# Kernel optimization log

Measured on AMD Instinct MI355X. Metric: run time of the kernel, lower is better.

The kernel has to match this reference:

```python
import jax, jax.numpy as jnp
import numpy as np

BINS = 100
ALPHA = 0.1

def entropy_batch(h):
    # Faithful to torch: histogram path is detached (done in numpy in original).
    h = jax.lax.stop_gradient(h)
    B, D = h.shape
    hp = h - jnp.min(h, axis=1, keepdims=True)
    hn = hp / jnp.max(hp, axis=1, keepdims=True)  # normalized to [0, 1]
    # np.histogram with `bins` uniform bins over [0,1]; rightmost edge inclusive -> clip
    idx = jnp.clip(jnp.floor(hn * BINS).astype(jnp.int32), 0, BINS - 1)
    rows = jnp.arange(B)[:, None]
    counts = jnp.zeros((B, BINS), jnp.float32).at[rows, idx].add(1.0)
    px = counts / jnp.float32(D)
    safe = jnp.where(px > 0, px, 1.0)
    ent = -jnp.sum(px * jnp.log(safe), axis=1) + jnp.log(jnp.float32(BINS))
    return jnp.mean(ent)

def setup_inputs() -> dict:
    key = jax.random.key(0)
    ks = jax.random.split(key, 8)
    B = 65536
    archi = [246, 246, 246, 246, 246, 246]
    dims = [784] + archi
    inp = {"x": jax.random.normal(ks[0], (B, 1, 28, 28), jnp.float32)}
    for i in range(6):
        inp[f"W{i+1}"] = 0.01 * jax.random.normal(ks[i + 1], (dims[i + 1], dims[i]), jnp.float32)
        inp[f"b{i+1}"] = jnp.zeros((dims[i + 1],), jnp.float32)
    inp["W7"] = 0.01 * jax.random.normal(ks[7], (10, archi[-1]), jnp.float32)
    inp["b7"] = jnp.zeros((10,), jnp.float32)
    return inp

def reference(x, W1, b1, W2, b2, W3, b3, W4, b4, W5, b5, W6, b6, W7, b7):
    h = x.reshape(-1, 784)
    Hs = []
    for W, b in ((W1, b1), (W2, b2), (W3, b3), (W4, b4), (W5, b5), (W6, b6)):
        h = jax.nn.leaky_relu(h @ W.T + b, negative_slope=ALPHA)
        Hs.append(entropy_batch(h))
    logits = jax.nn.relu(h @ W7.T + b7)
    out = jax.nn.log_softmax(logits, axis=1)
    return (out, Hs[0], Hs[1], Hs[2], Hs[3], Hs[4], Hs[5])
```

## Files before the change

kernel.cpp:

```cpp
#include <hip/hip_runtime.h>
#include <cstdint>
#include <cmath>

#define BATCH 65536
#define NREAL 246
#define NPAD  256
#define K1    784
#define K1PAD 832
#define BINS  100
#define ALPHA 0.1f
#define RB    128
#define NBLK  (BATCH/RB)

typedef __bf16 bf16x8 __attribute__((ext_vector_type(8)));
typedef __bf16 bf16x4 __attribute__((ext_vector_type(4)));
typedef float  f32x4  __attribute__((ext_vector_type(4)));

__global__ __launch_bounds__(256)
void pad_weights(const float* __restrict__ W1, const float* __restrict__ W2,
                 const float* __restrict__ W3, const float* __restrict__ W4,
                 const float* __restrict__ W5, const float* __restrict__ W6,
                 const float* __restrict__ W7,
                 __bf16* __restrict__ W1p, __bf16* __restrict__ Wp,
                 __bf16* __restrict__ W7p)
{
    int tid = blockIdx.x * 256 + threadIdx.x;
    const int n1 = NPAD * K1PAD;
    const int n2 = 5 * NPAD * NPAD;
    if (tid < n1) {
        int row = tid / K1PAD;
        int k   = tid - row * K1PAD;
        W1p[tid] = (__bf16)((row < NREAL && k < K1) ? W1[row * K1 + k] : 0.0f);
    } else if (tid < n1 + n2) {
        int t = tid - n1;
        int wsel = t >> 16;
        int idx  = t & 65535;
        int row  = idx >> 8, k = idx & 255;
        const float* W = (wsel == 0) ? W2 : (wsel == 1) ? W3 : (wsel == 2) ? W4
                        : (wsel == 3) ? W5 : W6;
        Wp[t] = (__bf16)((row < NREAL && k < NREAL) ? W[row * NREAL + k] : 0.0f);
    } else if (tid < n1 + n2 + 16 * NPAD) {
        int t = tid - n1 - n2;
        int row = t >> 8, k = t & 255;
        W7p[t] = (__bf16)((row < 10 && k < NREAL) ? W7[row * NREAL + k] : 0.0f);
    }
}

__global__ __launch_bounds__(512)
void mega(const float* __restrict__ x,
          const __bf16* __restrict__ W1p,
          const __bf16* __restrict__ Wp,
          const __bf16* __restrict__ W7p,
          const float* __restrict__ b1, const float* __restrict__ b2,
          const float* __restrict__ b3, const float* __restrict__ b4,
          const float* __restrict__ b5, const float* __restrict__ b6,
          const float* __restrict__ b7,
          float* __restrict__ out, float* __restrict__ partial)
{
    __shared__ __bf16 Hs[RB * NPAD];
    __shared__ char   aux[32768];
    char* Hb = (char*)Hs;

    const int tid = threadIdx.x;
    const int w = tid >> 6, l = tid & 63;
    const int lane16 = l & 15, lane4 = l >> 4;
    const int wr = (w >> 2) * 64;
    const int wc = (w & 3) * 64;
    const int m0 = blockIdx.x * RB;
    const int swzA = (lane16 & 7) << 4;

    f32x4 acc[4][4];
#pragma unroll
    for (int i = 0; i < 4; ++i)
#pragma unroll
        for (int j = 0; j < 4; ++j) acc[i][j] = f32x4{0.f, 0.f, 0.f, 0.f};

    auto loadB = [&](bf16x8 (&dst)[2][4], const __bf16* Bbase, int Kb, int kt) {
#pragma unroll
        for (int kk = 0; kk < 2; ++kk)
#pragma unroll
            for (int j = 0; j < 4; ++j) {
                int col = wc + j * 16 + lane16;
                dst[kk][j] = *(const bf16x8*)(Bbase + (size_t)col * Kb + kt * 64 + kk * 32 + lane4 * 8);
            }
    };

    const int srow = tid >> 2, skq = tid & 3;
    auto stageIssue = [&](int kt, float4 (&xs)[4]) {
        int k0 = kt * 64 + skq * 16;
        if (k0 + 16 <= K1) {
            const float* gx = x + (size_t)(m0 + srow) * K1 + k0;
#pragma unroll
            for (int q = 0; q < 4; ++q) xs[q] = *(const float4*)(gx + q * 4);
        } else {
#pragma unroll
            for (int q = 0; q < 4; ++q) xs[q] = float4{0.f, 0.f, 0.f, 0.f};
        }
    };
    auto stageWrite = [&](int pdst, const float4 (&xs)[4]) {
        char* Ab = aux + pdst * 16384;
        bf16x8 h0, h1;
        h0[0]=(__bf16)xs[0].x; h0[1]=(__bf16)xs[0].y; h0[2]=(__bf16)xs[0].z; h0[3]=(__bf16)xs[0].w;
        h0[4]=(__bf16)xs[1].x; h0[5]=(__bf16)xs[1].y; h0[6]=(__bf16)xs[1].z; h0[7]=(__bf16)xs[1].w;
        h1[0]=(__bf16)xs[2].x; h1[1]=(__bf16)xs[2].y; h1[2]=(__bf16)xs[2].z; h1[3]=(__bf16)xs[2].w;
        h1[4]=(__bf16)xs[3].x; h1[5]=(__bf16)xs[3].y; h1[6]=(__bf16)xs[3].z; h1[7]=(__bf16)xs[3].w;
        int s = (srow & 7) << 4;
        int base = srow * 128;
        *(bf16x8*)(Ab + base + ((skq * 32)      ^ s)) = h0;
        *(bf16x8*)(Ab + base + ((skq * 32 + 16) ^ s)) = h1;
    };

    auto computeL1 = [&](const bf16x8 (&bfr)[2][4], int pcur) {
        const char* Ab = aux + pcur * 16384;
#pragma unroll
        for (int kk = 0; kk < 2; ++kk) {
            bf16x8 af[4];
#pragma unroll
            for (int i = 0; i < 4; ++i) {
                int row = wr + i * 16 + lane16;
                int kb = kk * 64 + lane4 * 16;
                af[i] = *(const bf16x8*)(Ab + row * 128 + (kb ^ swzA));
            }
#pragma unroll
            for (int i = 0; i < 4; ++i)
#pragma unroll
                for (int j = 0; j < 4; ++j)
                    acc[i][j] = __builtin_amdgcn_mfma_f32_16x16x32_bf16(af[i], bfr[kk][j], acc[i][j], 0, 0, 0);
        }
    };

    auto computeMid = [&](const bf16x8 (&bfr)[2][4], int kt) {
#pragma unroll
        for (int kk = 0; kk < 2; ++kk) {
            bf16x8 af[4];
#pragma unroll
            for (int i = 0; i < 4; ++i) {
                int row = wr + i * 16 + lane16;
                int kb = kt * 128 + kk * 64 + lane4 * 16;
                af[i] = *(const bf16x8*)(Hb + row * 512 + (kb ^ swzA));
            }
#pragma unroll
            for (int i = 0; i < 4; ++i)
#pragma unroll
                for (int j = 0; j < 4; ++j)
                    acc[i][j] = __builtin_amdgcn_mfma_f32_16x16x32_bf16(af[i], bfr[kk][j], acc[i][j], 0, 0, 0);
        }
    };

    auto epilogue = [&](const float* bias) {
#pragma unroll
        for (int j = 0; j < 4; ++j) {
            int col = wc + j * 16 + lane16;
            bool cv = col < NREAL;
            float bv = cv ? bias[col] : 0.0f;
#pragma unroll
            for (int i = 0; i < 4; ++i) {
#pragma unroll
                for (int r = 0; r < 4; ++r) {
                    int row = wr + i * 16 + lane4 * 4 + r;
                    float v = acc[i][j][r] + bv;
                    v = v > 0.0f ? v : ALPHA * v;
                    *(__bf16*)(Hb + row * 512 + ((col * 2) ^ ((row & 7) << 4))) =
                        cv ? (__bf16)v : (__bf16)0.0f;
                }
            }
        }
    };

    const float LN246 = logf(246.0f);

    auto entropy = [&](int li) {
        int*   hist = (int*)aux + w * 100;
        float* went = (float*)(aux + 3200);
        float* lut  = (float*)(aux + 3264);
        float wsum = 0.0f;
        for (int it = 0; it < 16; ++it) {
            int row = w * 16 + it;
            if (l < 50) { hist[l] = 0; hist[l + 50] = 0; }
            asm volatile("s_waitcnt lgkmcnt(0)" ::: "memory");
            int kb = (l * 8) ^ ((it & 7) << 4);
            bf16x4 hv = *(const bf16x4*)(Hb + row * 512 + kb);
            float v[4];
#pragma unroll
            for (int e = 0; e < 4; ++e) v[e] = (float)hv[e];
            int c0 = l * 4;
            float mn = 1e30f, mx = -1e30f;
#pragma unroll
            for (int e = 0; e < 4; ++e)
                if (c0 + e < NREAL) { mn = fminf(mn, v[e]); mx = fmaxf(mx, v[e]); }
#pragma unroll
            for (int off = 32; off; off >>= 1) {
                mn = fminf(mn, __shfl_xor(mn, off, 64));
                mx = fmaxf(mx, __shfl_xor(mx, off, 64));
            }
            float range = mx - mn;
            float rr = (range > 0.0f) ? 1.0f / range : 0.0f;
#pragma unroll
            for (int e = 0; e < 4; ++e) {
                if (c0 + e < NREAL) {
                    int idx = (int)floorf((v[e] - mn) * rr * 100.0f);
                    idx = idx < 0 ? 0 : (idx > BINS - 1 ? BINS - 1 : idx);
                    atomicAdd(&hist[idx], 1);
                }
            }
            asm volatile("s_waitcnt lgkmcnt(0)" ::: "memory");
            float S = lut[hist[l]];
            if (l < BINS - 64) S += lut[hist[64 + l]];
#pragma unroll
            for (int off = 32; off; off >>= 1) S += __shfl_xor(S, off, 64);
            wsum += LN246 - S * (1.0f / 246.0f);
        }
        if (l == 0) went[w] = wsum;
        __syncthreads();
        if (tid == 0) {
            float s = 0.0f;
#pragma unroll
            for (int q = 0; q < 8; ++q) s += went[q];
            partial[li * NBLK + blockIdx.x] = s;
        }
    };

    {
        bf16x8 bA[2][4], bB[2][4];
        loadB(bA, W1p, K1PAD, 0);
        { float4 xs[4]; stageIssue(0, xs); stageWrite(0, xs); }
        for (int n = 0; n < 6; ++n) {
            int kt = 2 * n;
            __syncthreads();
            { float4 xn[4];
              stageIssue(kt + 1, xn); loadB(bB, W1p, K1PAD, kt + 1);
              computeL1(bA, 0);
              stageWrite(1, xn); }
            __syncthreads();
            { float4 xn[4];
              stageIssue(kt + 2, xn); loadB(bA, W1p, K1PAD, kt + 2);
              computeL1(bB, 1);
              stageWrite(0, xn); }
        }
        __syncthreads();
        computeL1(bA, 0);
    }
    __syncthreads();
    {
        float* lut = (float*)(aux + 3264);
        for (int c = tid; c < 247; c += 512) lut[c] = (c > 0) ? (float)c * logf((float)c) : 0.0f;
    }
    epilogue(b1);
    __syncthreads();
    entropy(0);

    const float* bsel[5] = {b2, b3, b4, b5, b6};
    for (int li = 0; li < 5; ++li) {
        const __bf16* Bp = Wp + (size_t)li * (NPAD * NPAD);
#pragma unroll
        for (int i = 0; i < 4; ++i)
#pragma unroll
            for (int j = 0; j < 4; ++j) acc[i][j] = f32x4{0.f, 0.f, 0.f, 0.f};

        bf16x8 mA[2][4], mB[2][4];
        loadB(mA, Bp, NPAD, 0);
        loadB(mB, Bp, NPAD, 1);  computeMid(mA, 0);
        loadB(mA, Bp, NPAD, 2);  computeMid(mB, 1);
        loadB(mB, Bp, NPAD, 3);  computeMid(mA, 2);
                                 computeMid(mB, 3);
        __syncthreads();
        epilogue(bsel[li]);
        __syncthreads();
        entropy(li + 1);
    }

    {
        f32x4 hacc = f32x4{0.f, 0.f, 0.f, 0.f};
#pragma unroll
        for (int kt = 0; kt < 8; ++kt) {
            int row = w * 16 + lane16;
            int kb = kt * 64 + lane4 * 16;
            bf16x8 af = *(const bf16x8*)(Hb + row * 512 + (kb ^ swzA));
            bf16x8 bf = *(const bf16x8*)(W7p + (size_t)lane16 * NPAD + kt * 32 + lane4 * 8);
            hacc = __builtin_amdgcn_mfma_f32_16x16x32_bf16(af, bf, hacc, 0, 0, 0);
        }
        float bv = (lane16 < 10) ? b7[lane16] : 0.0f;
#pragma unroll
        for (int r = 0; r < 4; ++r) {
            float lg = fmaxf(hacc[r] + bv, 0.0f);
            float vm = (lane16 < 10) ? lg : -1e30f;
#pragma unroll
            for (int off = 8; off; off >>= 1) vm = fmaxf(vm, __shfl_xor(vm, off, 64));
            float ex = (lane16 < 10) ? expf(lg - vm) : 0.0f;
#pragma unroll
            for (int off = 8; off; off >>= 1) ex += __shfl_xor(ex, off, 64);
            float ls = vm + logf(ex);
            if (lane16 < 10) {
                int grow = m0 + w * 16 + lane4 * 4 + r;
                out[(size_t)grow * 10 + lane16] = lg - ls;
            }
        }
    }
}

__global__ __launch_bounds__(256)
void reduce_kernel(const float* __restrict__ partial, float* __restrict__ out)
{
    __shared__ float s[256];
    const int li = blockIdx.x, tid = threadIdx.x;
    float a = partial[li * NBLK + tid] + partial[li * NBLK + 256 + tid];
    s[tid] = a;
    __syncthreads();
    for (int st = 128; st; st >>= 1) {
        if (tid < st) s[tid] += s[tid + st];
        __syncthreads();
    }
    if (tid == 0)
        out[(size_t)BATCH * 10 + li] = s[0] / (float)BATCH + logf((float)BINS);
}

extern "C" void kernel_launch(void* const* d_in, const int* in_sizes, int n_in,
                              void* d_out, int out_size, void* d_ws, size_t ws_size,
                              hipStream_t stream)
{
    (void)in_sizes; (void)n_in; (void)out_size; (void)ws_size;

    const float* x  = (const float*)d_in[0];
    const float* W1 = (const float*)d_in[1];
    const float* b1 = (const float*)d_in[2];
    const float* W2 = (const float*)d_in[3];
    const float* b2 = (const float*)d_in[4];
    const float* W3 = (const float*)d_in[5];
    const float* b3 = (const float*)d_in[6];
    const float* W4 = (const float*)d_in[7];
    const float* b4 = (const float*)d_in[8];
    const float* W5 = (const float*)d_in[9];
    const float* b5 = (const float*)d_in[10];
    const float* W6 = (const float*)d_in[11];
    const float* b6 = (const float*)d_in[12];
    const float* W7 = (const float*)d_in[13];
    const float* b7 = (const float*)d_in[14];

    char* ws = (char*)d_ws;
    __bf16* W1p = (__bf16*)(ws);
    __bf16* Wp  = (__bf16*)(ws + 425984);
    __bf16* W7p = (__bf16*)(ws + 1081344);
    float*  partial = (float*)(ws + 1089536);
    float*  out = (float*)d_out;

    pad_weights<<<2128, 256, 0, stream>>>(W1, W2, W3, W4, W5, W6, W7, W1p, Wp, W7p);
    mega<<<NBLK, 512, 0, stream>>>(x, W1p, Wp, W7p, b1, b2, b3, b4, b5, b6, b7, out, partial);
    reduce_kernel<<<6, 256, 0, stream>>>(partial, out);
}
```

Before: 354.5 us.

## Halve rows per block, fuse row min/max into epilogue, parallelize entropy histograms

Rows per block drop from 128 to 64, so each block needs less LDS and fewer accumulator registers, and the launch bound now asks for more resident blocks per CU. The GEMM epilogue now computes per-row min/max via shuffles and stores them in LDS, so the entropy pass no longer rescans each row. Each wave then builds 8 row histograms at once instead of looping serially, with one shared sync per layer and the per-layer partial writes deferred to the end. The W1 stream is loaded directly per k-step instead of being double-buffered in registers, which may expose more global latency. The result is twice as many blocks and partial sums, and the reduction kernel is updated to match.

```diff
diff --git a/kernel.cpp b/kernel.cpp
--- a/kernel.cpp
+++ b/kernel.cpp
@@ -9,12 +9,21 @@
 #define K1PAD 832
 #define BINS  100
 #define ALPHA 0.1f
-#define RB    128
+#define RB    64
 #define NBLK  (BATCH/RB)
 
 typedef __bf16 bf16x8 __attribute__((ext_vector_type(8)));
 typedef __bf16 bf16x4 __attribute__((ext_vector_type(4)));
 typedef float  f32x4  __attribute__((ext_vector_type(4)));
+
+#define OFF_HS     0
+#define OFF_STAGE  32768
+#define OFF_HIST   32768
+#define OFF_MN     58368
+#define OFF_MX     59392
+#define OFF_LUT    60416
+#define OFF_WENT   61440
+#define LDS_TOTAL  61696
 
 __global__ __launch_bounds__(256)
 void pad_weights(const float* __restrict__ W1, const float* __restrict__ W2,
@@ -46,7 +55,7 @@
     }
 }
 
-__global__ __launch_bounds__(512)
+__global__ __launch_bounds__(512, 4)
 void mega(const float* __restrict__ x,
           const __bf16* __restrict__ W1p,
           const __bf16* __restrict__ Wp,
@@ -57,193 +66,162 @@
           const float* __restrict__ b7,
           float* __restrict__ out, float* __restrict__ partial)
 {
-    __shared__ __bf16 Hs[RB * NPAD];
-    __shared__ char   aux[32768];
-    char* Hb = (char*)Hs;
+    __shared__ char smem[LDS_TOTAL];
+    char*  Hb    = smem + OFF_HS;
+    float* rowmn = (float*)(smem + OFF_MN);
+    float* rowmx = (float*)(smem + OFF_MX);
+    float* lut   = (float*)(smem + OFF_LUT);
+    float* went  = (float*)(smem + OFF_WENT);
 
     const int tid = threadIdx.x;
     const int w = tid >> 6, l = tid & 63;
     const int lane16 = l & 15, lane4 = l >> 4;
-    const int wr = (w >> 2) * 64;
+    const int wr = (w >> 2) * 32;
     const int wc = (w & 3) * 64;
     const int m0 = blockIdx.x * RB;
-    const int swzA = (lane16 & 7) << 4;
-
-    f32x4 acc[4][4];
-#pragma unroll
-    for (int i = 0; i < 4; ++i)
+
+    if (tid > 0 && tid < 247) lut[tid] = (float)tid * logf((float)tid);
+    if (tid == 0) lut[0] = 0.0f;
+
+    f32x4 acc[2][4];
+#pragma unroll
+    for (int i = 0; i < 2; ++i)
 #pragma unroll
         for (int j = 0; j < 4; ++j) acc[i][j] = f32x4{0.f, 0.f, 0.f, 0.f};
 
-    auto loadB = [&](bf16x8 (&dst)[2][4], const __bf16* Bbase, int Kb, int kt) {
-#pragma unroll
-        for (int kk = 0; kk < 2; ++kk)
-#pragma unroll
-            for (int j = 0; j < 4; ++j) {
-                int col = wc + j * 16 + lane16;
-                dst[kk][j] = *(const bf16x8*)(Bbase + (size_t)col * Kb + kt * 64 + kk * 32 + lane4 * 8);
-            }
-    };
-
-    const int srow = tid >> 2, skq = tid & 3;
-    auto stageIssue = [&](int kt, float4 (&xs)[4]) {
-        int k0 = kt * 64 + skq * 16;
-        if (k0 + 16 <= K1) {
-            const float* gx = x + (size_t)(m0 + srow) * K1 + k0;
-#pragma unroll
-            for (int q = 0; q < 4; ++q) xs[q] = *(const float4*)(gx + q * 4);
-        } else {
-#pragma unroll
-            for (int q = 0; q < 4; ++q) xs[q] = float4{0.f, 0.f, 0.f, 0.f};
-        }
-    };
-    auto stageWrite = [&](int pdst, const float4 (&xs)[4]) {
-        char* Ab = aux + pdst * 16384;
-        bf16x8 h0, h1;
-        h0[0]=(__bf16)xs[0].x; h0[1]=(__bf16)xs[0].y; h0[2]=(__bf16)xs[0].z; h0[3]=(__bf16)xs[0].w;
-        h0[4]=(__bf16)xs[1].x; h0[5]=(__bf16)xs[1].y; h0[6]=(__bf16)xs[1].z; h0[7]=(__bf16)xs[1].w;
-        h1[0]=(__bf16)xs[2].x; h1[1]=(__bf16)xs[2].y; h1[2]=(__bf16)xs[2].z; h1[3]=(__bf16)xs[2].w;
-        h1[4]=(__bf16)xs[3].x; h1[5]=(__bf16)xs[3].y; h1[6]=(__bf16)xs[3].z; h1[7]=(__bf16)xs[3].w;
-        int s = (srow & 7) << 4;
-        int base = srow * 128;
-        *(bf16x8*)(Ab + base + ((skq * 32)      ^ s)) = h0;
-        *(bf16x8*)(Ab + base + ((skq * 32 + 16) ^ s)) = h1;
-    };
-
-    auto computeL1 = [&](const bf16x8 (&bfr)[2][4], int pcur) {
-        const char* Ab = aux + pcur * 16384;
-#pragma unroll
-        for (int kk = 0; kk < 2; ++kk) {
-            bf16x8 af[4];
-#pragma unroll
-            for (int i = 0; i < 4; ++i) {
-                int row = wr + i * 16 + lane16;
-                int kb = kk * 64 + lane4 * 16;
-                af[i] = *(const bf16x8*)(Ab + row * 128 + (kb ^ swzA));
-            }
-#pragma unroll
-            for (int i = 0; i < 4; ++i)
-#pragma unroll
-                for (int j = 0; j < 4; ++j)
-                    acc[i][j] = __builtin_amdgcn_mfma_f32_16x16x32_bf16(af[i], bfr[kk][j], acc[i][j], 0, 0, 0);
-        }
-    };
-
-    auto computeMid = [&](const bf16x8 (&bfr)[2][4], int kt) {
-#pragma unroll
-        for (int kk = 0; kk < 2; ++kk) {
-            bf16x8 af[4];
-#pragma unroll
-            for (int i = 0; i < 4; ++i) {
-                int row = wr + i * 16 + lane16;
-                int kb = kt * 128 + kk * 64 + lane4 * 16;
-                af[i] = *(const bf16x8*)(Hb + row * 512 + (kb ^ swzA));
-            }
-#pragma unroll
-            for (int i = 0; i < 4; ++i)
-#pragma unroll
-                for (int j = 0; j < 4; ++j)
-                    acc[i][j] = __builtin_amdgcn_mfma_f32_16x16x32_bf16(af[i], bfr[kk][j], acc[i][j], 0, 0, 0);
-        }
-    };
-
     auto epilogue = [&](const float* bias) {
+        float bv[4];
 #pragma unroll
         for (int j = 0; j < 4; ++j) {
             int col = wc + j * 16 + lane16;
-            bool cv = col < NREAL;
-            float bv = cv ? bias[col] : 0.0f;
-#pragma unroll
-            for (int i = 0; i < 4; ++i) {
-#pragma unroll
-                for (int r = 0; r < 4; ++r) {
-                    int row = wr + i * 16 + lane4 * 4 + r;
-                    float v = acc[i][j][r] + bv;
+            bv[j] = (col < NREAL) ? bias[col] : 0.0f;
+        }
+#pragma unroll
+        for (int i = 0; i < 2; ++i) {
+#pragma unroll
+            for (int rr = 0; rr < 4; ++rr) {
+                int row = wr + i * 16 + lane4 * 4 + rr;
+                int swz = (row & 7) << 4;
+                float mn = 1e30f, mx = -1e30f;
+#pragma unroll
+                for (int j = 0; j < 4; ++j) {
+                    int col = wc + j * 16 + lane16;
+                    bool cv = col < NREAL;
+                    float v = acc[i][j][rr] + bv[j];
                     v = v > 0.0f ? v : ALPHA * v;
-                    *(__bf16*)(Hb + row * 512 + ((col * 2) ^ ((row & 7) << 4))) =
-                        cv ? (__bf16)v : (__bf16)0.0f;
+                    *(__bf16*)(Hb + row * 512 + ((col * 2) ^ swz)) = cv ? (__bf16)v : (__bf16)0.0f;
+                    mn = fminf(mn, cv ? v : 1e30f);
+                    mx = fmaxf(mx, cv ? v : -1e30f);
+                }
+#pragma unroll
+                for (int off = 1; off < 16; off <<= 1) {
+                    mn = fminf(mn, __shfl_xor(mn, off, 64));
+                    mx = fmaxf(mx, __shfl_xor(mx, off, 64));
+                }
+                if (lane16 == 0) {
+                    rowmn[row * 4 + (w & 3)] = mn;
+                    rowmx[row * 4 + (w & 3)] = mx;
                 }
             }
         }
     };
 
-    const float LN246 = logf(246.0f);
-
     auto entropy = [&](int li) {
-        int*   hist = (int*)aux + w * 100;
-        float* went = (float*)(aux + 3200);
-        float* lut  = (float*)(aux + 3264);
-        float wsum = 0.0f;
-        for (int it = 0; it < 16; ++it) {
-            int row = w * 16 + it;
-            if (l < 50) { hist[l] = 0; hist[l + 50] = 0; }
-            asm volatile("s_waitcnt lgkmcnt(0)" ::: "memory");
-            int kb = (l * 8) ^ ((it & 7) << 4);
-            bf16x4 hv = *(const bf16x4*)(Hb + row * 512 + kb);
-            float v[4];
-#pragma unroll
-            for (int e = 0; e < 4; ++e) v[e] = (float)hv[e];
-            int c0 = l * 4;
-            float mn = 1e30f, mx = -1e30f;
-#pragma unroll
-            for (int e = 0; e < 4; ++e)
-                if (c0 + e < NREAL) { mn = fminf(mn, v[e]); mx = fmaxf(mx, v[e]); }
-#pragma unroll
-            for (int off = 32; off; off >>= 1) {
-                mn = fminf(mn, __shfl_xor(mn, off, 64));
-                mx = fmaxf(mx, __shfl_xor(mx, off, 64));
-            }
-            float range = mx - mn;
-            float rr = (range > 0.0f) ? 1.0f / range : 0.0f;
+        int* histW = (int*)(smem + OFF_HIST) + w * 800;
+        f32x4 m4 = *(const f32x4*)(rowmn + l * 4);
+        f32x4 x4 = *(const f32x4*)(rowmx + l * 4);
+        float mnl = fminf(fminf(m4[0], m4[1]), fminf(m4[2], m4[3]));
+        float mxl = fmaxf(fmaxf(x4[0], x4[1]), fmaxf(x4[2], x4[3]));
+        float rgl = mxl - mnl;
+        float rsl = (rgl > 0.0f) ? 100.0f / rgl : 0.0f;
+#pragma unroll
+        for (int t = 0; t < 13; ++t) { int b = t * 64 + l; if (b < 800) histW[b] = 0; }
+        asm volatile("s_waitcnt lgkmcnt(0)" ::: "memory");
+        const int c0 = l * 4;
+#pragma unroll
+        for (int rr = 0; rr < 8; ++rr) {
+            int row = w * 8 + rr;
+            float rm = __shfl(mnl, row, 64);
+            float rs = __shfl(rsl, row, 64);
+            bf16x4 hv = *(const bf16x4*)(Hb + row * 512 + ((c0 * 2) ^ ((row & 7) << 4)));
 #pragma unroll
             for (int e = 0; e < 4; ++e) {
                 if (c0 + e < NREAL) {
-                    int idx = (int)floorf((v[e] - mn) * rr * 100.0f);
+                    int idx = (int)floorf(((float)hv[e] - rm) * rs);
                     idx = idx < 0 ? 0 : (idx > BINS - 1 ? BINS - 1 : idx);
-                    atomicAdd(&hist[idx], 1);
-                }
-            }
-            asm volatile("s_waitcnt lgkmcnt(0)" ::: "memory");
-            float S = lut[hist[l]];
-            if (l < BINS - 64) S += lut[hist[64 + l]];
-#pragma unroll
-            for (int off = 32; off; off >>= 1) S += __shfl_xor(S, off, 64);
-            wsum += LN246 - S * (1.0f / 246.0f);
-        }
-        if (l == 0) went[w] = wsum;
-        __syncthreads();
-        if (tid == 0) {
-            float s = 0.0f;
-#pragma unroll
-            for (int q = 0; q < 8; ++q) s += went[q];
-            partial[li * NBLK + blockIdx.x] = s;
-        }
+                    atomicAdd(&histW[rr * 100 + idx], 1);
+                }
+            }
+        }
+        asm volatile("s_waitcnt lgkmcnt(0)" ::: "memory");
+        float S = 0.0f;
+        const int rbase = (l >> 3) * 100, tb = (l & 7) * 13;
+#pragma unroll
+        for (int t = 0; t < 13; ++t) {
+            int b = tb + t;
+            if (b < 100) S += lut[histW[rbase + b]];
+        }
+#pragma unroll
+        for (int off = 1; off < 64; off <<= 1) S += __shfl_xor(S, off, 64);
+        if (l == 0) went[w * 6 + li] = 8.0f * logf(246.0f) - S * (1.0f / 246.0f);
     };
 
     {
-        bf16x8 bA[2][4], bB[2][4];
-        loadB(bA, W1p, K1PAD, 0);
-        { float4 xs[4]; stageIssue(0, xs); stageWrite(0, xs); }
-        for (int n = 0; n < 6; ++n) {
-            int kt = 2 * n;
+        const int srow = tid >> 3;
+        const int skc  = (tid & 7) * 8;
+        float4 xr0, xr1;
+        auto issueX = [&](int kt) {
+            int k0 = kt * 64 + skc;
+            if (k0 < K1) {
+                const float* gx = x + (size_t)(m0 + srow) * K1 + k0;
+                xr0 = *(const float4*)gx;
+                xr1 = *(const float4*)(gx + 4);
+            } else {
+                xr0 = float4{0.f,0.f,0.f,0.f};
+                xr1 = float4{0.f,0.f,0.f,0.f};
+            }
+        };
+        auto writeX = [&](int buf) {
+            bf16x8 h;
+            h[0]=(__bf16)xr0.x; h[1]=(__bf16)xr0.y; h[2]=(__bf16)xr0.z; h[3]=(__bf16)xr0.w;
+            h[4]=(__bf16)xr1.x; h[5]=(__bf16)xr1.y; h[6]=(__bf16)xr1.z; h[7]=(__bf16)xr1.w;
+            char* st = smem + OFF_STAGE + buf * 8192;
+            *(bf16x8*)(st + srow * 128 + ((skc * 2) ^ ((srow & 7) << 4))) = h;
+        };
+        auto l1step = [&](int kt, int buf) {
+            const char* st = smem + OFF_STAGE + buf * 8192;
+#pragma unroll
+            for (int kk = 0; kk < 2; ++kk) {
+                bf16x8 bfr[4];
+#pragma unroll
+                for (int j = 0; j < 4; ++j)
+                    bfr[j] = *(const bf16x8*)(W1p + (size_t)(wc + j * 16 + lane16) * K1PAD
+                                              + kt * 64 + kk * 32 + lane4 * 8);
+                bf16x8 af[2];
+#pragma unroll
+                for (int i = 0; i < 2; ++i) {
+                    int row = wr + i * 16 + lane16;
+                    af[i] = *(const bf16x8*)(st + row * 128 + ((kk * 64 + lane4 * 16) ^ ((row & 7) << 4)));
+                }
+#pragma unroll
+                for (int i = 0; i < 2; ++i)
+#pragma unroll
+                    for (int j = 0; j < 4; ++j)
+                        acc[i][j] = __builtin_amdgcn_mfma_f32_16x16x32_bf16(af[i], bfr[j], acc[i][j], 0, 0, 0);
+            }
+        };
+
+        issueX(0);
+        writeX(0);
+        issueX(1);
+        for (int kt = 0; kt < 13; ++kt) {
             __syncthreads();
-            { float4 xn[4];
-              stageIssue(kt + 1, xn); loadB(bB, W1p, K1PAD, kt + 1);
-              computeL1(bA, 0);
-              stageWrite(1, xn); }
-            __syncthreads();
-            { float4 xn[4];
-              stageIssue(kt + 2, xn); loadB(bA, W1p, K1PAD, kt + 2);
-              computeL1(bB, 1);
-              stageWrite(0, xn); }
-        }
-        __syncthreads();
-        computeL1(bA, 0);
-    }
-    __syncthreads();
-    {
-        float* lut = (float*)(aux + 3264);
-        for (int c = tid; c < 247; c += 512) lut[c] = (c > 0) ? (float)c * logf((float)c) : 0.0f;
+            if (kt < 12) {
+                writeX((kt + 1) & 1);
+                if (kt < 11) issueX(kt + 2);
+            }
+            l1step(kt, kt & 1);
+        }
     }
     epilogue(b1);
     __syncthreads();
@@ -253,29 +231,44 @@
     for (int li = 0; li < 5; ++li) {
         const __bf16* Bp = Wp + (size_t)li * (NPAD * NPAD);
 #pragma unroll
-        for (int i = 0; i < 4; ++i)
+        for (int i = 0; i < 2; ++i)
 #pragma unroll
             for (int j = 0; j < 4; ++j) acc[i][j] = f32x4{0.f, 0.f, 0.f, 0.f};
-
-        bf16x8 mA[2][4], mB[2][4];
-        loadB(mA, Bp, NPAD, 0);
-        loadB(mB, Bp, NPAD, 1);  computeMid(mA, 0);
-        loadB(mA, Bp, NPAD, 2);  computeMid(mB, 1);
-        loadB(mB, Bp, NPAD, 3);  computeMid(mA, 2);
-                                 computeMid(mB, 3);
+#pragma unroll
+        for (int kt = 0; kt < 4; ++kt) {
+#pragma unroll
+            for (int kk = 0; kk < 2; ++kk) {
+                bf16x8 bfr[4];
+#pragma unroll
+                for (int j = 0; j < 4; ++j)
+                    bfr[j] = *(const bf16x8*)(Bp + (size_t)(wc + j * 16 + lane16) * NPAD
+                                              + kt * 64 + kk * 32 + lane4 * 8);
+                bf16x8 af[2];
+#pragma unroll
+                for (int i = 0; i < 2; ++i) {
+                    int row = wr + i * 16 + lane16;
+                    af[i] = *(const bf16x8*)(Hb + row * 512
+                              + ((kt * 128 + kk * 64 + lane4 * 16) ^ ((row & 7) << 4)));
+                }
+#pragma unroll
+                for (int i = 0; i < 2; ++i)
+#pragma unroll
+                    for (int j = 0; j < 4; ++j)
+                        acc[i][j] = __builtin_amdgcn_mfma_f32_16x16x32_bf16(af[i], bfr[j], acc[i][j], 0, 0, 0);
+            }
+        }
         __syncthreads();
         epilogue(bsel[li]);
         __syncthreads();
         entropy(li + 1);
     }
 
-    {
+    if (w < 4) {
         f32x4 hacc = f32x4{0.f, 0.f, 0.f, 0.f};
+        int row = w * 16 + lane16;
 #pragma unroll
         for (int kt = 0; kt < 8; ++kt) {
-            int row = w * 16 + lane16;
-            int kb = kt * 64 + lane4 * 16;
-            bf16x8 af = *(const bf16x8*)(Hb + row * 512 + (kb ^ swzA));
+            bf16x8 af = *(const bf16x8*)(Hb + row * 512 + ((kt * 64 + lane4 * 16) ^ ((row & 7) << 4)));
             bf16x8 bf = *(const bf16x8*)(W7p + (size_t)lane16 * NPAD + kt * 32 + lane4 * 8);
             hacc = __builtin_amdgcn_mfma_f32_16x16x32_bf16(af, bf, hacc, 0, 0, 0);
         }
@@ -296,6 +289,14 @@
             }
         }
     }
+
+    __syncthreads();
+    if (tid < 6) {
+        float s = 0.0f;
+#pragma unroll
+        for (int q = 0; q < 8; ++q) s += went[q * 6 + tid];
+        partial[tid * NBLK + blockIdx.x] = s;
+    }
 }
 
 __global__ __launch_bounds__(256)
@@ -303,7 +304,8 @@
 {
     __shared__ float s[256];
     const int li = blockIdx.x, tid = threadIdx.x;
-    float a = partial[li * NBLK + tid] + partial[li * NBLK + 256 + tid];
+    float a = 0.0f;
+    for (int i = tid; i < NBLK; i += 256) a += partial[li * NBLK + i];
     s[tid] = a;
     __syncthreads();
     for (int st = 128; st; st >>= 1) {
```

Result: slower. 388.9 us (+9.7%).
